# Optimization experiments

Measured on AMD Instinct MI355X. Metric: run time of the kernel, lower is better.

Reference implementation:

```python
import jax, jax.numpy as jnp
import numpy as np

NUM_TASKS, IN_SIZE, OUT_SIZE, N_ROWS = 64, 512, 512, 2048


def setup_inputs() -> dict:
    key = jax.random.key(0)
    k_x, k_t, k_w = jax.random.split(key, 3)
    inputs = jax.random.normal(k_x, (N_ROWS, IN_SIZE), dtype=jnp.float32)
    task_ids = jax.random.randint(k_t, (N_ROWS,), 0, NUM_TASKS, dtype=jnp.int64)
    # in_size == out_size path: identity + N(0, 0.03) perturbation per task
    W = (jnp.eye(IN_SIZE, OUT_SIZE, dtype=jnp.float32)[None]
         + 0.03 * jax.random.normal(k_w, (NUM_TASKS, IN_SIZE, OUT_SIZE), dtype=jnp.float32))
    return {"inputs": inputs, "task_ids": task_ids, "W": W}


def reference(inputs, task_ids, W):
    # Gather the full per-row weight matrix then batched vector-matrix multiply,
    # faithful to torch.einsum('ni,nio->no', inputs, W[task_ids]).
    aligned = W[task_ids]                       # [I, in, out]
    return jnp.einsum("ni,nio->no", inputs, aligned)  # [I, out]
```

## Files before the change

kernel.cpp:

```cpp
#include <hip/hip_runtime.h>


#define NDIM 512
#define KDIM 512
#define NCOL 32
#define LISTCAP 256

typedef _Float16 f16x8 __attribute__((ext_vector_type(8)));
typedef float    f32x4 __attribute__((ext_vector_type(4)));
typedef int      i32x4 __attribute__((ext_vector_type(4)));

__global__ __launch_bounds__(1024, 4) void k_big(
    const float* __restrict__ x,
    const int*   __restrict__ tids,
    const float* __restrict__ W,
    float*       __restrict__ out,
    int n_rows)
{
    const int tid  = threadIdx.x;
    const int lane = tid & 63;
    const int wv   = tid >> 6;
    const int ml   = lane & 15;
    const int q    = lane >> 4;
    const int sc4  = (lane & 7) * 4;
    const int ol   = lane >> 3;

    const int u    = wv >> 2;
    const int sub  = wv & 3;

    const int bid   = blockIdx.x;
    const int task  = (bid & 7) | ((bid >> 5) << 3);
    const int chunk = ((bid >> 3) & 3) * 4 + u;
    const int c0    = chunk * NCOL;

    __shared__ __align__(16) _Float16 Wt[4][NCOL * KDIM];
    __shared__ unsigned short rl[4][LISTCAP];

    _Float16*       Wm  = &Wt[u][0];
    unsigned short* rlm = &rl[u][0];

    const float* Wg = W + (size_t)task * KDIM * NDIM + c0;

    i32x4 tvv[8];
    #pragma unroll
    for (int cb = 0; cb < 8; ++cb) {
        const int r4 = cb * 256 + lane * 4;
        if (r4 + 3 < n_rows) {
            tvv[cb] = *(const i32x4*)(tids + r4);
        } else {
            #pragma unroll
            for (int j = 0; j < 4; ++j)
                tvv[cb][j] = (r4 + j < n_rows) ? tids[r4 + j] : -1;
        }
    }

    float4 wr[8];
    auto issueS = [&](int s) {
        const size_t kb = (size_t)(ol + 8 * s) * 8;
        #pragma unroll
        for (int j = 0; j < 8; ++j)
            wr[j] = *(const float4*)(Wg + (kb + j) * NDIM + sc4);
    };
    auto stageS = [&](int s) {
        const int oct = ol + 8 * s;
        #pragma unroll
        for (int j2 = 0; j2 < 4; ++j2) {
            f16x8 h8;
            #pragma unroll
            for (int j = 0; j < 8; ++j)
                h8[j] = (_Float16)(((const float*)&wr[j])[j2]);
            const int c  = sc4 + j2;
            const int po = oct ^ (c & 7);
            *(f16x8*)&Wm[c * KDIM + po * 8] = h8;
        }
    };

    issueS(2 * sub);

    int cnt = 0;
    #pragma unroll
    for (int cb = 0; cb < 8; ++cb) {
        #pragma unroll
        for (int j = 0; j < 4; ++j) {
            const bool m = (tvv[cb][j] == task);
            const unsigned long long bal = __ballot(m);
            const int rank = __popcll(bal & ((1ull << lane) - 1ull));
            const int slot = cnt + rank;
            if (m && slot < LISTCAP) rlm[slot] = (unsigned short)(cb * 256 + lane * 4 + j);
            cnt += __popcll(bal);
        }
    }
    if (cnt > LISTCAP) cnt = LISTCAP;

    stageS(2 * sub);
    issueS(2 * sub + 1);
    stageS(2 * sub + 1);

    __syncthreads();

    f32x4 xqA[8], xqB[8];
    auto issueQ = [&](const float* xr, int qi, f32x4 (&xq)[8]) {
        #pragma unroll
        for (int s = 0; s < 4; ++s) {
            const int ks = qi * 4 + s;
            xq[2 * s]     = *(const f32x4*)(xr + ks * 32 + q * 8);
            xq[2 * s + 1] = *(const f32x4*)(xr + ks * 32 + q * 8 + 4);
        }
    };
    auto cvtQ = [&](const f32x4 (&xq)[8], f16x8* pf) {
        #pragma unroll
        for (int s = 0; s < 4; ++s) {
            f16x8 af;
            const float* a0 = (const float*)&xq[2 * s];
            #pragma unroll
            for (int j = 0; j < 8; ++j) af[j] = (_Float16)a0[j];
            pf[s] = af;
        }
    };
    auto mmaH = [&](int half, const f16x8* pf, f32x4& a0, f32x4& a1) {
        #pragma unroll
        for (int ksl = 0; ksl < 8; ++ksl) {
            const int oct = (half * 8 + ksl) * 4 + q;
            {
                const int po = oct ^ (ml & 7);
                const f16x8 bf = *(const f16x8*)&Wm[ml * KDIM + po * 8];
                a0 = __builtin_amdgcn_mfma_f32_16x16x32_f16(pf[ksl], bf, a0, 0, 0, 0);
            }
            {
                const int cB = 16 + ml;
                const int po = oct ^ (cB & 7);
                const f16x8 bf = *(const f16x8*)&Wm[cB * KDIM + po * 8];
                a1 = __builtin_amdgcn_mfma_f32_16x16x32_f16(pf[ksl], bf, a1, 0, 0, 0);
            }
        }
    };

    for (int g0 = sub * 16; g0 < cnt; g0 += 64) {
        const int idx = g0 + ml;
        const int row = rlm[(idx < cnt) ? idx : (cnt - 1)];
        const float* xr = x + (size_t)row * KDIM;

        f16x8 pafA[8], pafB[8];
        f32x4 acc0 = {}, acc1 = {};

        issueQ(xr, 0, xqA);
        issueQ(xr, 1, xqB);
        cvtQ(xqA, pafA);     issueQ(xr, 2, xqA);
        cvtQ(xqB, pafA + 4); issueQ(xr, 3, xqB);
        mmaH(0, pafA, acc0, acc1);
        cvtQ(xqA, pafB);
        cvtQ(xqB, pafB + 4);
        mmaH(1, pafB, acc0, acc1);

        #pragma unroll
        for (int rg = 0; rg < 4; ++rg) {
            const int pos = g0 + q * 4 + rg;
            if (pos < cnt) {
                float* op = out + (size_t)rlm[pos] * NDIM + c0 + ml;
                op[0]  = acc0[rg];
                op[16] = acc1[rg];
            }
        }
    }
}

extern "C" void kernel_launch(void* const* d_in, const int* in_sizes, int n_in,
                              void* d_out, int out_size, void* d_ws, size_t ws_size,
                              hipStream_t stream) {
    const float* x    = (const float*)d_in[0];
    const int*   tids = (const int*)d_in[1];
    const float* W    = (const float*)d_in[2];
    float*       out  = (float*)d_out;
    const int n_rows  = in_sizes[1];

    k_big<<<dim3(256), dim3(1024), 0, stream>>>(x, tids, W, out, n_rows);
}
```

Before: 126.2 us.

## Use one block per task with K-slab double-buffered weight staging

Launches one 512-thread block per task instead of four column-split blocks per task. Each block streams the task's full weight matrix through LDS in 64-deep K slabs with double buffering, and each wave computes 16 rows by 256 columns with 16 accumulators. The aim is to cut redundant row-list construction and to overlap weight loading with MFMA work. The risks are only 64 blocks on a 256-CU GPU, which leaves most of the machine idle, and weights being re-streamed for every 64-row group.

```diff
diff --git a/kernel.cpp b/kernel.cpp
--- a/kernel.cpp
+++ b/kernel.cpp
@@ -1,16 +1,17 @@
 #include <hip/hip_runtime.h>
 
 
-#define NDIM 512
-#define KDIM 512
-#define NCOL 32
-#define LISTCAP 256
+#define NDIM  512
+#define KDIM  512
+#define SLABK 64
+#define NSLAB 8
+#define LISTCAP 2048
 
 typedef _Float16 f16x8 __attribute__((ext_vector_type(8)));
 typedef float    f32x4 __attribute__((ext_vector_type(4)));
 typedef int      i32x4 __attribute__((ext_vector_type(4)));
 
-__global__ __launch_bounds__(1024, 4) void k_big(
+__global__ __launch_bounds__(512, 2) void k_task(
     const float* __restrict__ x,
     const int*   __restrict__ tids,
     const float* __restrict__ W,
@@ -22,24 +23,47 @@
     const int wv   = tid >> 6;
     const int ml   = lane & 15;
     const int q    = lane >> 4;
-    const int sc4  = (lane & 7) * 4;
-    const int ol   = lane >> 3;
+    const int rg   = wv >> 1;
+    const int cq   = wv & 1;
 
-    const int u    = wv >> 2;
-    const int sub  = wv & 3;
+    const int cg   = tid & 127;
+    const int ot   = tid >> 7;
 
-    const int bid   = blockIdx.x;
-    const int task  = (bid & 7) | ((bid >> 5) << 3);
-    const int chunk = ((bid >> 3) & 3) * 4 + u;
-    const int c0    = chunk * NCOL;
+    const int task = blockIdx.x;
+    const float* Wg = W + (size_t)task * KDIM * NDIM;
 
-    __shared__ __align__(16) _Float16 Wt[4][NCOL * KDIM];
-    __shared__ unsigned short rl[4][LISTCAP];
+    __shared__ __align__(16) _Float16 Wt[2][NDIM * SLABK];
+    __shared__ unsigned short rl[LISTCAP];
 
-    _Float16*       Wm  = &Wt[u][0];
-    unsigned short* rlm = &rl[u][0];
+    float4 wb[16];
+    auto issueSlab = [&](int s) {
+        const float* base = Wg + (size_t)(s * SLABK) * NDIM + cg * 4;
+        #pragma unroll
+        for (int st = 0; st < 2; ++st) {
+            const int oct = ot + st * 4;
+            #pragma unroll
+            for (int j = 0; j < 8; ++j)
+                wb[st * 8 + j] = *(const float4*)(base + (size_t)(oct * 8 + j) * NDIM);
+        }
+    };
+    auto stageSlab = [&](int b) {
+        #pragma unroll
+        for (int st = 0; st < 2; ++st) {
+            const int oct = ot + st * 4;
+            #pragma unroll
+            for (int j2 = 0; j2 < 4; ++j2) {
+                f16x8 h8;
+                #pragma unroll
+                for (int j = 0; j < 8; ++j)
+                    h8[j] = (_Float16)(((const float*)&wb[st * 8 + j])[j2]);
+                const int c  = cg * 4 + j2;
+                const int po = oct ^ (c & 7);
+                *(f16x8*)&Wt[b][c * SLABK + po * 8] = h8;
+            }
+        }
+    };
 
-    const float* Wg = W + (size_t)task * KDIM * NDIM + c0;
+    issueSlab(0);
 
     i32x4 tvv[8];
     #pragma unroll
@@ -54,29 +78,6 @@
         }
     }
 
-    float4 wr[8];
-    auto issueS = [&](int s) {
-        const size_t kb = (size_t)(ol + 8 * s) * 8;
-        #pragma unroll
-        for (int j = 0; j < 8; ++j)
-            wr[j] = *(const float4*)(Wg + (kb + j) * NDIM + sc4);
-    };
-    auto stageS = [&](int s) {
-        const int oct = ol + 8 * s;
-        #pragma unroll
-        for (int j2 = 0; j2 < 4; ++j2) {
-            f16x8 h8;
-            #pragma unroll
-            for (int j = 0; j < 8; ++j)
-                h8[j] = (_Float16)(((const float*)&wr[j])[j2]);
-            const int c  = sc4 + j2;
-            const int po = oct ^ (c & 7);
-            *(f16x8*)&Wm[c * KDIM + po * 8] = h8;
-        }
-    };
-
-    issueS(2 * sub);
-
     int cnt = 0;
     #pragma unroll
     for (int cb = 0; cb < 8; ++cb) {
@@ -86,80 +87,85 @@
             const unsigned long long bal = __ballot(m);
             const int rank = __popcll(bal & ((1ull << lane) - 1ull));
             const int slot = cnt + rank;
-            if (m && slot < LISTCAP) rlm[slot] = (unsigned short)(cb * 256 + lane * 4 + j);
+            if (m && slot < LISTCAP) rl[slot] = (unsigned short)(cb * 256 + lane * 4 + j);
             cnt += __popcll(bal);
         }
     }
-    if (cnt > LISTCAP) cnt = LISTCAP;
 
-    stageS(2 * sub);
-    issueS(2 * sub + 1);
-    stageS(2 * sub + 1);
+    if (cnt == 0) return;
 
-    __syncthreads();
+    for (int g0B = 0; g0B < cnt; g0B += 64) {
+        if (g0B > 0) issueSlab(0);
 
-    f32x4 xqA[8], xqB[8];
-    auto issueQ = [&](const float* xr, int qi, f32x4 (&xq)[8]) {
+        const int gpos = g0B + rg * 16 + ml;
+        const int row  = rl[(gpos < cnt) ? gpos : (cnt - 1)];
+        const float* xr = x + (size_t)row * KDIM;
+
+        f32x4 acc[16];
         #pragma unroll
-        for (int s = 0; s < 4; ++s) {
-            const int ks = qi * 4 + s;
-            xq[2 * s]     = *(const f32x4*)(xr + ks * 32 + q * 8);
-            xq[2 * s + 1] = *(const f32x4*)(xr + ks * 32 + q * 8 + 4);
-        }
-    };
-    auto cvtQ = [&](const f32x4 (&xq)[8], f16x8* pf) {
+        for (int ct = 0; ct < 16; ++ct) acc[ct] = (f32x4){};
+
+        stageSlab(0);
+        issueSlab(1);
+        asm volatile("s_waitcnt lgkmcnt(0)" ::: "memory");
+        __builtin_amdgcn_s_barrier();
+        __builtin_amdgcn_sched_barrier(0);
+
         #pragma unroll
-        for (int s = 0; s < 4; ++s) {
-            f16x8 af;
-            const float* a0 = (const float*)&xq[2 * s];
+        for (int s = 0; s < NSLAB; ++s) {
+            const int b = s & 1;
+
+            f32x4 xa[4];
             #pragma unroll
-            for (int j = 0; j < 8; ++j) af[j] = (_Float16)a0[j];
-            pf[s] = af;
-        }
-    };
-    auto mmaH = [&](int half, const f16x8* pf, f32x4& a0, f32x4& a1) {
-        #pragma unroll
-        for (int ksl = 0; ksl < 8; ++ksl) {
-            const int oct = (half * 8 + ksl) * 4 + q;
-            {
-                const int po = oct ^ (ml & 7);
-                const f16x8 bf = *(const f16x8*)&Wm[ml * KDIM + po * 8];
-                a0 = __builtin_amdgcn_mfma_f32_16x16x32_f16(pf[ksl], bf, a0, 0, 0, 0);
+            for (int ks = 0; ks < 2; ++ks) {
+                xa[2 * ks]     = *(const f32x4*)(xr + s * SLABK + ks * 32 + q * 8);
+                xa[2 * ks + 1] = *(const f32x4*)(xr + s * SLABK + ks * 32 + q * 8 + 4);
             }
-            {
-                const int cB = 16 + ml;
-                const int po = oct ^ (cB & 7);
-                const f16x8 bf = *(const f16x8*)&Wm[cB * KDIM + po * 8];
-                a1 = __builtin_amdgcn_mfma_f32_16x16x32_f16(pf[ksl], bf, a1, 0, 0, 0);
+            f16x8 af[2];
+            #pragma unroll
+            for (int ks = 0; ks < 2; ++ks) {
+                f16x8 t8;
+                const float* a0 = (const float*)&xa[2 * ks];
+                #pragma unroll
+                for (int j = 0; j < 8; ++j) t8[j] = (_Float16)a0[j];
+                af[ks] = t8;
+            }
+
+            #pragma unroll
+            for (int ks = 0; ks < 2; ++ks) {
+                #pragma unroll
+                for (int ct = 0; ct < 16; ++ct) {
+                    const int cB = cq * 256 + ct * 16 + ml;
+                    const int po = (ks * 4 + q) ^ (cB & 7);
+                    const f16x8 bf = *(const f16x8*)&Wt[b][cB * SLABK + po * 8];
+                    acc[ct] = __builtin_amdgcn_mfma_f32_16x16x32_f16(af[ks], bf, acc[ct], 0, 0, 0);
+                }
+            }
+
+            if (s + 1 < NSLAB) {
+                stageSlab((s + 1) & 1);
+                if (s + 2 < NSLAB) issueSlab(s + 2);
+                asm volatile("s_waitcnt lgkmcnt(0)" ::: "memory");
+                __builtin_amdgcn_s_barrier();
+                __builtin_amdgcn_sched_barrier(0);
             }
         }
-    };
-
-    for (int g0 = sub * 16; g0 < cnt; g0 += 64) {
-        const int idx = g0 + ml;
-        const int row = rlm[(idx < cnt) ? idx : (cnt - 1)];
-        const float* xr = x + (size_t)row * KDIM;
-
-        f16x8 pafA[8], pafB[8];
-        f32x4 acc0 = {}, acc1 = {};
-
-        issueQ(xr, 0, xqA);
-        issueQ(xr, 1, xqB);
-        cvtQ(xqA, pafA);     issueQ(xr, 2, xqA);
-        cvtQ(xqB, pafA + 4); issueQ(xr, 3, xqB);
-        mmaH(0, pafA, acc0, acc1);
-        cvtQ(xqA, pafB);
-        cvtQ(xqB, pafB + 4);
-        mmaH(1, pafB, acc0, acc1);
 
         #pragma unroll
-        for (int rg = 0; rg < 4; ++rg) {
-            const int pos = g0 + q * 4 + rg;
+        for (int rgi = 0; rgi < 4; ++rgi) {
+            const int pos = g0B + rg * 16 + q * 4 + rgi;
             if (pos < cnt) {
-                float* op = out + (size_t)rlm[pos] * NDIM + c0 + ml;
-                op[0]  = acc0[rg];
-                op[16] = acc1[rg];
+                float* op = out + (size_t)rl[pos] * NDIM + cq * 256 + ml;
+                #pragma unroll
+                for (int ct = 0; ct < 16; ++ct)
+                    op[ct * 16] = acc[ct][rgi];
             }
+        }
+
+        if (g0B + 64 < cnt) {
+            asm volatile("s_waitcnt lgkmcnt(0)" ::: "memory");
+            __builtin_amdgcn_s_barrier();
+            __builtin_amdgcn_sched_barrier(0);
         }
     }
 }
@@ -173,5 +179,5 @@
     float*       out  = (float*)d_out;
     const int n_rows  = in_sizes[1];
 
-    k_big<<<dim3(256), dim3(1024), 0, stream>>>(x, tids, W, out, n_rows);
+    k_task<<<dim3(64), dim3(512), 0, stream>>>(x, tids, W, out, n_rows);
 }
```

Result: slower. 183.4 us (+45.3%).
